# Performance work log

Hardware: AMD Instinct MI355X
Metric: run time of the kernel (lower is better)

The kernel has to match this reference:

```python
import jax, jax.numpy as jnp
import numpy as np

EPS = 1e-8

def setup_inputs() -> dict:
    key = jax.random.key(0)
    x = jax.random.normal(key, (128, 1, 512, 512), dtype=jnp.float32)
    return {"x": x}

def reference(x) -> jnp.ndarray:
    # base_model is identity here; the module under study is the post-processing:
    # softplus, then per-sample divide by that sample's max (if max > 1e-8).
    pred = jax.nn.softplus(x)  # [B, C, H, W]
    # max over all non-batch dims, per sample
    sample_max = jnp.max(pred, axis=(1, 2, 3), keepdims=True)  # [B,1,1,1]
    safe_max = jnp.where(sample_max > EPS, sample_max, jnp.float32(1.0))
    return jnp.where(sample_max > EPS, pred / safe_max, pred)
```

## Files before the change

kernel.cpp:

```cpp
#include <hip/hip_runtime.h>
#include <math.h>


#define PER_SAMPLE (512 * 512)
#define F4_PER_SAMPLE (PER_SAMPLE / 4)
#define BLOCKS_PER_SAMPLE 16
#define THREADS 256
#define F4_PER_BLOCK (F4_PER_SAMPLE / BLOCKS_PER_SAMPLE)
#define F4_PER_THREAD (F4_PER_BLOCK / THREADS)
#define BATCH 4

typedef float f32x4 __attribute__((ext_vector_type(4)));

__device__ __forceinline__ float softplus_f(float x) {
    return fmaxf(x, 0.0f) + __logf(1.0f + __expf(-fabsf(x)));
}

__global__ __launch_bounds__(THREADS) void rawmax_kernel(
        const float* __restrict__ x, float* __restrict__ partials) {
    const int sample = blockIdx.x / BLOCKS_PER_SAMPLE;
    const int part   = blockIdx.x % BLOCKS_PER_SAMPLE;
    const int t      = threadIdx.x;

    const f32x4* x4 = (const f32x4*)x +
        (size_t)sample * F4_PER_SAMPLE + (size_t)part * F4_PER_BLOCK;

    float m = -INFINITY;
#pragma unroll
    for (int b = 0; b < F4_PER_THREAD / BATCH; ++b) {
        f32x4 v[BATCH];
#pragma unroll
        for (int j = 0; j < BATCH; ++j)
            v[j] = x4[(size_t)(b * BATCH + j) * THREADS + t];
#pragma unroll
        for (int j = 0; j < BATCH; ++j)
            m = fmaxf(m, fmaxf(fmaxf(v[j].x, v[j].y), fmaxf(v[j].z, v[j].w)));
    }

#pragma unroll
    for (int off = 32; off > 0; off >>= 1)
        m = fmaxf(m, __shfl_down(m, off, 64));

    __shared__ float wmax[THREADS / 64];
    if ((t & 63) == 0) wmax[t >> 6] = m;
    __syncthreads();

    if (t == 0) {
        float bm = wmax[0];
#pragma unroll
        for (int w = 1; w < THREADS / 64; ++w) bm = fmaxf(bm, wmax[w]);
        partials[blockIdx.x] = bm;
    }
}

__global__ __launch_bounds__(THREADS) void scale_kernel(
        const float* __restrict__ x, const float* __restrict__ partials,
        float* __restrict__ out) {
    const int sample = blockIdx.x / BLOCKS_PER_SAMPLE;
    const int part   = blockIdx.x % BLOCKS_PER_SAMPLE;
    const int t      = threadIdx.x;

    __shared__ float s_scale;
    if (t < 64) {
        float p = (t < BLOCKS_PER_SAMPLE)
                    ? partials[sample * BLOCKS_PER_SAMPLE + t] : -INFINITY;
#pragma unroll
        for (int off = 8; off > 0; off >>= 1)
            p = fmaxf(p, __shfl_xor(p, off, 64));
        if (t == 0) {
            float m = softplus_f(p);
            s_scale = (m > 1e-8f) ? (1.0f / m) : 1.0f;
        }
    }
    __syncthreads();
    const float scale = s_scale;

    const size_t base =
        (size_t)sample * F4_PER_SAMPLE + (size_t)part * F4_PER_BLOCK;
    const f32x4* x4 = (const f32x4*)x + base;
    f32x4* o4       = (f32x4*)out + base;

#pragma unroll
    for (int b = 0; b < F4_PER_THREAD / BATCH; ++b) {
        f32x4 v[BATCH];
#pragma unroll
        for (int j = 0; j < BATCH; ++j)
            v[j] = x4[(size_t)(b * BATCH + j) * THREADS + t];
#pragma unroll
        for (int j = 0; j < BATCH; ++j) {
            f32x4 r;
            r.x = softplus_f(v[j].x) * scale;
            r.y = softplus_f(v[j].y) * scale;
            r.z = softplus_f(v[j].z) * scale;
            r.w = softplus_f(v[j].w) * scale;
            __builtin_nontemporal_store(
                r, &o4[(size_t)(b * BATCH + j) * THREADS + t]);
        }
    }
}

extern "C" void kernel_launch(void* const* d_in, const int* in_sizes, int n_in,
                              void* d_out, int out_size, void* d_ws, size_t ws_size,
                              hipStream_t stream) {
    const float* x  = (const float*)d_in[0];
    float* out      = (float*)d_out;
    float* partials = (float*)d_ws;

    const int n_total   = in_sizes[0];
    const int n_samples = n_total / PER_SAMPLE;
    const int grid      = n_samples * BLOCKS_PER_SAMPLE;

    rawmax_kernel<<<grid, THREADS, 0, stream>>>(x, partials);
    scale_kernel<<<grid, THREADS, 0, stream>>>(x, partials, out);
}
```

Before: 249.4 us.

## Fuse max and scale passes into one kernel with per-sample atomic barrier

Merges the two passes into one kernel. Each block keeps its 64 KB slice in registers, publishes its partial max through an order-preserving atomicMax key and a per-sample arrival counter, then spins until all blocks of its sample arrive before scaling. This removes the second full read of the input from HBM and one kernel launch. It adds a small init kernel and relies on all 16 blocks of a sample being co-resident. A timeout falls back to recomputing the max from global memory, and heavy register use may limit occupancy.

Measured after the change: 403.0 us. 1.62x slower.

```diff
diff --git a/kernel.cpp b/kernel.cpp
--- a/kernel.cpp
+++ b/kernel.cpp
@@ -8,7 +8,6 @@
 #define THREADS 256
 #define F4_PER_BLOCK (F4_PER_SAMPLE / BLOCKS_PER_SAMPLE)
 #define F4_PER_THREAD (F4_PER_BLOCK / THREADS)
-#define BATCH 4
 
 typedef float f32x4 __attribute__((ext_vector_type(4)));
 
@@ -16,32 +15,48 @@
     return fmaxf(x, 0.0f) + __logf(1.0f + __expf(-fabsf(x)));
 }
 
-__global__ __launch_bounds__(THREADS) void rawmax_kernel(
-        const float* __restrict__ x, float* __restrict__ partials) {
+__device__ __forceinline__ unsigned key_of(float f) {
+    unsigned u = __float_as_uint(f);
+    return (u & 0x80000000u) ? ~u : (u | 0x80000000u);
+}
+__device__ __forceinline__ float float_of_key(unsigned k) {
+    unsigned u = (k & 0x80000000u) ? (k ^ 0x80000000u) : ~k;
+    return __uint_as_float(u);
+}
+
+__global__ void init_ws(unsigned* __restrict__ ws, int n_samples) {
+    for (int i = threadIdx.x; i < 2 * n_samples; i += blockDim.x) ws[i] = 0u;
+}
+
+__global__ __launch_bounds__(THREADS, 4) void fused_kernel(
+        const float* __restrict__ x, unsigned* __restrict__ ws,
+        float* __restrict__ out, int n_samples) {
     const int sample = blockIdx.x / BLOCKS_PER_SAMPLE;
     const int part   = blockIdx.x % BLOCKS_PER_SAMPLE;
     const int t      = threadIdx.x;
 
-    const f32x4* x4 = (const f32x4*)x +
+    const size_t base =
         (size_t)sample * F4_PER_SAMPLE + (size_t)part * F4_PER_BLOCK;
+    const f32x4* x4 = (const f32x4*)x + base;
+    f32x4* o4       = (f32x4*)out + base;
+
+    f32x4 v[F4_PER_THREAD];
+#pragma unroll
+    for (int j = 0; j < F4_PER_THREAD; ++j)
+        v[j] = x4[(size_t)j * THREADS + t];
 
     float m = -INFINITY;
 #pragma unroll
-    for (int b = 0; b < F4_PER_THREAD / BATCH; ++b) {
-        f32x4 v[BATCH];
-#pragma unroll
-        for (int j = 0; j < BATCH; ++j)
-            v[j] = x4[(size_t)(b * BATCH + j) * THREADS + t];
-#pragma unroll
-        for (int j = 0; j < BATCH; ++j)
-            m = fmaxf(m, fmaxf(fmaxf(v[j].x, v[j].y), fmaxf(v[j].z, v[j].w)));
-    }
+    for (int j = 0; j < F4_PER_THREAD; ++j)
+        m = fmaxf(m, fmaxf(fmaxf(v[j].x, v[j].y), fmaxf(v[j].z, v[j].w)));
 
 #pragma unroll
     for (int off = 32; off > 0; off >>= 1)
         m = fmaxf(m, __shfl_down(m, off, 64));
 
     __shared__ float wmax[THREADS / 64];
+    __shared__ float s_max;
+    __shared__ int   s_ok;
     if ((t & 63) == 0) wmax[t >> 6] = m;
     __syncthreads();
 
@@ -49,67 +64,69 @@
         float bm = wmax[0];
 #pragma unroll
         for (int w = 1; w < THREADS / 64; ++w) bm = fmaxf(bm, wmax[w]);
-        partials[blockIdx.x] = bm;
-    }
-}
 
-__global__ __launch_bounds__(THREADS) void scale_kernel(
-        const float* __restrict__ x, const float* __restrict__ partials,
-        float* __restrict__ out) {
-    const int sample = blockIdx.x / BLOCKS_PER_SAMPLE;
-    const int part   = blockIdx.x % BLOCKS_PER_SAMPLE;
-    const int t      = threadIdx.x;
+        unsigned* keys = ws;
+        unsigned* cnts = ws + n_samples;
+        atomicMax(&keys[sample], key_of(bm));
+        __hip_atomic_fetch_add(&cnts[sample], 1u,
+                               __ATOMIC_RELEASE, __HIP_MEMORY_SCOPE_AGENT);
 
-    __shared__ float s_scale;
-    if (t < 64) {
-        float p = (t < BLOCKS_PER_SAMPLE)
-                    ? partials[sample * BLOCKS_PER_SAMPLE + t] : -INFINITY;
-#pragma unroll
-        for (int off = 8; off > 0; off >>= 1)
-            p = fmaxf(p, __shfl_xor(p, off, 64));
-        if (t == 0) {
-            float m = softplus_f(p);
-            s_scale = (m > 1e-8f) ? (1.0f / m) : 1.0f;
+        int spins = 0; int ok = 1;
+        while (__hip_atomic_load(&cnts[sample], __ATOMIC_ACQUIRE,
+                                 __HIP_MEMORY_SCOPE_AGENT)
+               < (unsigned)BLOCKS_PER_SAMPLE) {
+            __builtin_amdgcn_s_sleep(2);
+            if (++spins > 200000) { ok = 0; break; }
         }
+        s_ok = ok;
+        s_max = ok ? float_of_key(__hip_atomic_load(
+                        &keys[sample], __ATOMIC_RELAXED,
+                        __HIP_MEMORY_SCOPE_AGENT))
+                   : 0.0f;
     }
     __syncthreads();
-    const float scale = s_scale;
 
-    const size_t base =
-        (size_t)sample * F4_PER_SAMPLE + (size_t)part * F4_PER_BLOCK;
-    const f32x4* x4 = (const f32x4*)x + base;
-    f32x4* o4       = (f32x4*)out + base;
+    float raw_max = s_max;
+    if (!s_ok) {
+        const f32x4* s4 = (const f32x4*)x + (size_t)sample * F4_PER_SAMPLE;
+        float fm = -INFINITY;
+        for (int i = t; i < F4_PER_SAMPLE; i += THREADS) {
+            f32x4 w = s4[i];
+            fm = fmaxf(fm, fmaxf(fmaxf(w.x, w.y), fmaxf(w.z, w.w)));
+        }
+#pragma unroll
+        for (int off = 32; off > 0; off >>= 1)
+            fm = fmaxf(fm, __shfl_down(fm, off, 64));
+        if ((t & 63) == 0) wmax[t >> 6] = fm;
+        __syncthreads();
+        raw_max = fmaxf(fmaxf(wmax[0], wmax[1]), fmaxf(wmax[2], wmax[3]));
+    }
+
+    float mm    = softplus_f(raw_max);
+    float scale = (mm > 1e-8f) ? (1.0f / mm) : 1.0f;
 
 #pragma unroll
-    for (int b = 0; b < F4_PER_THREAD / BATCH; ++b) {
-        f32x4 v[BATCH];
-#pragma unroll
-        for (int j = 0; j < BATCH; ++j)
-            v[j] = x4[(size_t)(b * BATCH + j) * THREADS + t];
-#pragma unroll
-        for (int j = 0; j < BATCH; ++j) {
-            f32x4 r;
-            r.x = softplus_f(v[j].x) * scale;
-            r.y = softplus_f(v[j].y) * scale;
-            r.z = softplus_f(v[j].z) * scale;
-            r.w = softplus_f(v[j].w) * scale;
-            __builtin_nontemporal_store(
-                r, &o4[(size_t)(b * BATCH + j) * THREADS + t]);
-        }
+    for (int j = 0; j < F4_PER_THREAD; ++j) {
+        f32x4 r;
+        r.x = softplus_f(v[j].x) * scale;
+        r.y = softplus_f(v[j].y) * scale;
+        r.z = softplus_f(v[j].z) * scale;
+        r.w = softplus_f(v[j].w) * scale;
+        __builtin_nontemporal_store(r, &o4[(size_t)j * THREADS + t]);
     }
 }
 
 extern "C" void kernel_launch(void* const* d_in, const int* in_sizes, int n_in,
                               void* d_out, int out_size, void* d_ws, size_t ws_size,
                               hipStream_t stream) {
-    const float* x  = (const float*)d_in[0];
-    float* out      = (float*)d_out;
-    float* partials = (float*)d_ws;
+    const float* x = (const float*)d_in[0];
+    float* out     = (float*)d_out;
+    unsigned* ws   = (unsigned*)d_ws;
 
     const int n_total   = in_sizes[0];
     const int n_samples = n_total / PER_SAMPLE;
     const int grid      = n_samples * BLOCKS_PER_SAMPLE;
 
-    rawmax_kernel<<<grid, THREADS, 0, stream>>>(x, partials);
-    scale_kernel<<<grid, THREADS, 0, stream>>>(x, partials, out);
+    init_ws<<<1, 256, 0, stream>>>(ws, n_samples);
+    fused_kernel<<<grid, THREADS, 0, stream>>>(x, ws, out, n_samples);
 }
```

## Stage softplus as fp16 in output buffer to avoid re-reading input

Applied to the files above, without the earlier changes.

The first pass now computes softplus and writes it as fp16 into the first half of each chunk's slot in the output buffer, alongside the raw max. The second pass reads that fp16 staging data instead of the fp32 input, then scales it and writes fp32 in place. This replaces the second full fp32 read of x and the repeated transcendental work with a half-size write plus a half-size read. In exchange it loses precision to fp16 rounding of the prediction, and relies on each block reading its staged data before any of its fp32 stores overwrite it.

Result: slower. 258.2 us (+3.5%).

```diff
diff --git a/kernel.cpp b/kernel.cpp
--- a/kernel.cpp
+++ b/kernel.cpp
@@ -9,32 +9,43 @@
 #define F4_PER_BLOCK (F4_PER_SAMPLE / BLOCKS_PER_SAMPLE)
 #define F4_PER_THREAD (F4_PER_BLOCK / THREADS)
 #define BATCH 4
+#define NBATCH (F4_PER_THREAD / BATCH)
+#define SLOT_BYTES (F4_PER_BLOCK * 16)
 
-typedef float f32x4 __attribute__((ext_vector_type(4)));
+typedef float    f32x4 __attribute__((ext_vector_type(4)));
+typedef _Float16 f16x4 __attribute__((ext_vector_type(4)));
+typedef _Float16 f16x8 __attribute__((ext_vector_type(8)));
 
 __device__ __forceinline__ float softplus_f(float x) {
     return fmaxf(x, 0.0f) + __logf(1.0f + __expf(-fabsf(x)));
 }
 
-__global__ __launch_bounds__(THREADS) void rawmax_kernel(
-        const float* __restrict__ x, float* __restrict__ partials) {
-    const int sample = blockIdx.x / BLOCKS_PER_SAMPLE;
-    const int part   = blockIdx.x % BLOCKS_PER_SAMPLE;
-    const int t      = threadIdx.x;
+__global__ __launch_bounds__(THREADS) void pred_max_kernel(
+        const float* __restrict__ x, float* __restrict__ partials,
+        float* __restrict__ out) {
+    const int chunk = blockIdx.x;
+    const int t     = threadIdx.x;
 
-    const f32x4* x4 = (const f32x4*)x +
-        (size_t)sample * F4_PER_SAMPLE + (size_t)part * F4_PER_BLOCK;
+    const f32x4* x4 = (const f32x4*)x + (size_t)chunk * F4_PER_BLOCK;
+    f16x4* h4 = (f16x4*)((char*)out + (size_t)chunk * SLOT_BYTES);
 
     float m = -INFINITY;
 #pragma unroll
-    for (int b = 0; b < F4_PER_THREAD / BATCH; ++b) {
+    for (int b = 0; b < NBATCH; ++b) {
         f32x4 v[BATCH];
 #pragma unroll
         for (int j = 0; j < BATCH; ++j)
             v[j] = x4[(size_t)(b * BATCH + j) * THREADS + t];
 #pragma unroll
-        for (int j = 0; j < BATCH; ++j)
+        for (int j = 0; j < BATCH; ++j) {
             m = fmaxf(m, fmaxf(fmaxf(v[j].x, v[j].y), fmaxf(v[j].z, v[j].w)));
+            f16x4 h;
+            h.x = (_Float16)softplus_f(v[j].x);
+            h.y = (_Float16)softplus_f(v[j].y);
+            h.z = (_Float16)softplus_f(v[j].z);
+            h.w = (_Float16)softplus_f(v[j].w);
+            h4[(size_t)(b * BATCH + j) * THREADS + t] = h;
+        }
     }
 
 #pragma unroll
@@ -49,15 +60,14 @@
         float bm = wmax[0];
 #pragma unroll
         for (int w = 1; w < THREADS / 64; ++w) bm = fmaxf(bm, wmax[w]);
-        partials[blockIdx.x] = bm;
+        partials[chunk] = bm;
     }
 }
 
 __global__ __launch_bounds__(THREADS) void scale_kernel(
-        const float* __restrict__ x, const float* __restrict__ partials,
-        float* __restrict__ out) {
-    const int sample = blockIdx.x / BLOCKS_PER_SAMPLE;
-    const int part   = blockIdx.x % BLOCKS_PER_SAMPLE;
+        const float* __restrict__ partials, float* __restrict__ out) {
+    const int chunk  = blockIdx.x;
+    const int sample = chunk / BLOCKS_PER_SAMPLE;
     const int t      = threadIdx.x;
 
     __shared__ float s_scale;
@@ -68,34 +78,35 @@
         for (int off = 8; off > 0; off >>= 1)
             p = fmaxf(p, __shfl_xor(p, off, 64));
         if (t == 0) {
-            float m = softplus_f(p);
-            s_scale = (m > 1e-8f) ? (1.0f / m) : 1.0f;
+            float mm = softplus_f(p);
+            s_scale = (mm > 1e-8f) ? (1.0f / mm) : 1.0f;
         }
     }
+
+    const f16x8* hv = (const f16x8*)((const char*)out + (size_t)chunk * SLOT_BYTES);
+    f16x8 ph[8];
+#pragma unroll
+    for (int j = 0; j < 8; ++j)
+        ph[j] = hv[(size_t)j * THREADS + t];
+
     __syncthreads();
     const float scale = s_scale;
 
-    const size_t base =
-        (size_t)sample * F4_PER_SAMPLE + (size_t)part * F4_PER_BLOCK;
-    const f32x4* x4 = (const f32x4*)x + base;
-    f32x4* o4       = (f32x4*)out + base;
-
+    f32x4* o4 = (f32x4*)out + (size_t)chunk * F4_PER_BLOCK;
 #pragma unroll
-    for (int b = 0; b < F4_PER_THREAD / BATCH; ++b) {
-        f32x4 v[BATCH];
-#pragma unroll
-        for (int j = 0; j < BATCH; ++j)
-            v[j] = x4[(size_t)(b * BATCH + j) * THREADS + t];
-#pragma unroll
-        for (int j = 0; j < BATCH; ++j) {
-            f32x4 r;
-            r.x = softplus_f(v[j].x) * scale;
-            r.y = softplus_f(v[j].y) * scale;
-            r.z = softplus_f(v[j].z) * scale;
-            r.w = softplus_f(v[j].w) * scale;
-            __builtin_nontemporal_store(
-                r, &o4[(size_t)(b * BATCH + j) * THREADS + t]);
-        }
+    for (int j = 0; j < 8; ++j) {
+        f32x4 a, b;
+        a.x = (float)ph[j][0] * scale;
+        a.y = (float)ph[j][1] * scale;
+        a.z = (float)ph[j][2] * scale;
+        a.w = (float)ph[j][3] * scale;
+        b.x = (float)ph[j][4] * scale;
+        b.y = (float)ph[j][5] * scale;
+        b.z = (float)ph[j][6] * scale;
+        b.w = (float)ph[j][7] * scale;
+        const size_t f = (size_t)512 * j + 2 * t;
+        o4[f]     = a;
+        o4[f + 1] = b;
     }
 }
 
@@ -110,6 +121,6 @@
     const int n_samples = n_total / PER_SAMPLE;
     const int grid      = n_samples * BLOCKS_PER_SAMPLE;
 
-    rawmax_kernel<<<grid, THREADS, 0, stream>>>(x, partials);
-    scale_kernel<<<grid, THREADS, 0, stream>>>(x, partials, out);
+    pred_max_kernel<<<grid, THREADS, 0, stream>>>(x, partials, out);
+    scale_kernel<<<grid, THREADS, 0, stream>>>(partials, out);
 }
```
